# Kernel tuning notes

Measured on AMD Instinct MI355X. Metric: run time of the kernel, lower is better.

Reference implementation:

```python
import jax, jax.numpy as jnp
import numpy as np

B, H, L = 16, 512, 2048
N2 = 32  # d_state/2 complex modes
DT_MIN, DT_MAX = 1e-3, 1e-1


def setup_inputs() -> dict:
    key = jax.random.key(0)
    ks = jax.random.split(key, 8)
    u = jax.random.normal(ks[0], (B, H, L), dtype=jnp.float32)
    D = jax.random.normal(ks[1], (H,), dtype=jnp.float32)
    # log-uniform timescales in [DT_MIN, DT_MAX]
    r = jax.random.uniform(ks[2], (H,), dtype=jnp.float32)
    log_dt = (np.log(DT_MIN) + r * (np.log(DT_MAX) - np.log(DT_MIN))).astype(jnp.float32)
    C_re = jax.random.normal(ks[3], (H, N2), dtype=jnp.float32)
    C_im = jax.random.normal(ks[4], (H, N2), dtype=jnp.float32)
    W1 = jax.random.normal(ks[5], (L, 2 * H), dtype=jnp.float32) / np.float32(np.sqrt(L))
    b1 = jnp.zeros((2 * H,), dtype=jnp.float32)
    W2 = jax.random.normal(ks[6], (2 * H, H), dtype=jnp.float32) / np.float32(np.sqrt(2 * H))
    b2 = jnp.zeros((H,), dtype=jnp.float32)
    return {"u": u, "D": D, "log_dt": log_dt, "C_re": C_re, "C_im": C_im,
            "W1": W1, "b1": b1, "W2": W2, "b2": b2}


def _s4d_kernel(log_dt, C_re, C_im, length):
    # S4D-Lin: A_n = -1/2 + i*pi*n
    n = jnp.arange(N2, dtype=jnp.float32)
    A = -0.5 + 1j * jnp.pi * n                      # (N2,)
    dt = jnp.exp(log_dt)                             # (H,)
    dtA = dt[:, None] * A[None, :]                   # (H, N2)
    C = (C_re + 1j * C_im) * (jnp.exp(dtA) - 1.0) / A
    # Vandermonde: k[h, l] = 2 * Re sum_n C[h,n] * exp(dtA[h,n] * l)
    K = jnp.exp(dtA[:, :, None] * jnp.arange(length, dtype=jnp.float32))  # (H, N2, L)
    return 2.0 * jnp.einsum('hn,hnl->hl', C, K).real  # (H, L)


def reference(u, D, log_dt, C_re, C_im, W1, b1, W2, b2):
    # u: (B, H, L)
    k = _s4d_kernel(log_dt, C_re, C_im, L)           # (H, L)
    k_f = jnp.fft.rfft(k, n=2 * L, axis=-1)          # (H, L+1)
    u_f = jnp.fft.rfft(u, n=2 * L, axis=-1)          # (B, H, L+1)
    y = jnp.fft.irfft(u_f * k_f[None], n=2 * L, axis=-1)[..., :L]
    y = y + u * D[:, None]
    y = jax.nn.gelu(y, approximate=False)
    # keras Conv1D(k=1) / tanh / Dense applied to channels-first tensor:
    # dense over last axis L -> 2H, tanh, dense 2H -> H
    y = jnp.tanh(jnp.einsum('bhl,lf->bhf', y, W1) + b1)  # (B, H, 2H)
    y = jnp.einsum('bhf,fo->bho', y, W2) + b2            # (B, H, H)
    return y
```

## Files before the change

kernel.cpp:

```cpp
#include <hip/hip_runtime.h>
#include <math.h>

#define B_  16
#define H_  512
#define L_  2048
#define N2_ 32
#define NC_ 16
#define LC_ 128

typedef __attribute__((ext_vector_type(8))) short short8;
typedef __attribute__((ext_vector_type(4))) float f32x4;

__device__ __forceinline__ short f2bf(float x) {
    unsigned u = __builtin_bit_cast(unsigned, x);
    u += 0x7fffu + ((u >> 16) & 1u);
    return (short)(u >> 16);
}
__device__ __forceinline__ float bf2f(unsigned short s) {
    unsigned u = ((unsigned)s) << 16;
    return __builtin_bit_cast(float, u);
}

__global__ void k0_table(const float* __restrict__ log_dt,
                         const float* __restrict__ C_re,
                         const float* __restrict__ C_im,
                         float4* __restrict__ tab) {
    int idx = blockIdx.x * blockDim.x + threadIdx.x;
    if (idx >= H_ * N2_) return;
    int h = idx >> 5, n = idx & 31;
    float dt = expf(log_dt[h]);
    float e  = expf(-0.5f * dt);
    float th = 3.14159265358979323846f * (float)n * dt;
    float lr = e * cosf(th), li = e * sinf(th);
    float ar = -0.5f, ai = 3.14159265358979323846f * (float)n;
    float den = ar * ar + ai * ai;
    float x = lr - 1.0f, y = li;
    float nr = (x * ar + y * ai) / den;
    float ni = (y * ar - x * ai) / den;
    float cr = C_re[idx], ci = C_im[idx];
    tab[idx] = make_float4(lr, li, cr * nr - ci * ni, cr * ni + ci * nr);
}

__global__ void t0_pow(const float4* __restrict__ tab, float2* __restrict__ POW) {
    int t = blockIdx.x * 256 + threadIdx.x;
    if (t >= H_ * N2_) return;
    int h = t >> 5;
    float4 v = tab[t];
    float lr = v.x, li = v.y;
    float pr = 1.0f, pi = 0.0f;
    float2* base = POW + (size_t)h * 129 * N2_ + (t & 31);
    for (int m = 0; m <= 128; ++m) {
        base[(size_t)m * N2_] = make_float2(pr, pi);
        float npr = pr * lr - pi * li;
        float npi = pr * li + pi * lr;
        pr = npr; pi = npi;
    }
}

__global__ void t_ktab(const float4* __restrict__ tab, const float2* __restrict__ POW,
                       float* __restrict__ ktab) {
    int t = blockIdx.x * 256 + threadIdx.x;
    if (t >= H_ * 128) return;
    int h = t >> 7, m = t & 127;
    const float2* P = POW + (size_t)h * 129 * N2_ + (size_t)m * N2_;
    const float4* tb = tab + h * N2_;
    float s = 0.0f;
    for (int n = 0; n < N2_; ++n) {
        float2 p = P[n];
        float4 v = tb[n];
        s += v.z * p.x - v.w * p.y;
    }
    ktab[t] = 2.0f * s;
}

__global__ void __launch_bounds__(256)
t1_fill(const float4* __restrict__ tab, const float2* __restrict__ POW,
        const float* __restrict__ ktab, short* __restrict__ Psw,
        short* __restrict__ Vsw) {
    int t = blockIdx.x * 256 + threadIdx.x;
    int sub = t & 7;
    int rowg = t >> 3;
    int h = rowg / 320, row = rowg % 320;
    if (row < 192) {
        short8 s0, s1;
        if (row < 128) {
            int l = row;
#pragma unroll
            for (int mm = 0; mm < 8; ++mm) {
                int m0 = sub * 16 + mm, m1 = m0 + 8;
                s0[mm] = (m0 <= l) ? f2bf(ktab[h * 128 + (l - m0)]) : (short)0;
                s1[mm] = (m1 <= l) ? f2bf(ktab[h * 128 + (l - m1)]) : (short)0;
            }
        } else {
            int j = row - 128, nn = j >> 1, part = j & 1;
            const float2* P = POW + (size_t)h * 129 * N2_ + nn;
#pragma unroll
            for (int mm = 0; mm < 8; ++mm) {
                int m0 = sub * 16 + mm, m1 = m0 + 8;
                float2 p0 = P[(size_t)(127 - m0) * N2_];
                float2 p1 = P[(size_t)(127 - m1) * N2_];
                s0[mm] = f2bf(part ? p0.y : p0.x);
                s1[mm] = f2bf(part ? p1.y : p1.x);
            }
        }
        *(short8*)(Psw + ((size_t)(h * 16 + sub * 2 + 0) * 192 + row) * 8) = s0;
        *(short8*)(Psw + ((size_t)(h * 16 + sub * 2 + 1) * 192 + row) * 8) = s1;
    } else {
        int l = row - 192;
        const float2* P = POW + (size_t)h * 129 * N2_ + (size_t)(l + 1) * N2_;
        const float4* tb = tab + h * N2_;
        short8 s;
#pragma unroll
        for (int jj = 0; jj < 8; ++jj) {
            int j = sub * 8 + jj, nn = j >> 1;
            float2 p = P[nn];
            float4 cv = tb[nn];
            float re = cv.z * p.x - cv.w * p.y;
            float im = cv.z * p.y + cv.w * p.x;
            s[jj] = f2bf((j & 1) ? -2.0f * im : 2.0f * re);
        }
        *(short8*)(Vsw + ((size_t)(h * 8 + sub) * 128 + l) * 8) = s;
    }
}

__global__ void __launch_bounds__(256)
conv_mfma(const float* __restrict__ u, const short* __restrict__ Psw,
          float* __restrict__ E, short* __restrict__ Ybuf) {
    __shared__ short Ps[16 * 192 * 8];
    __shared__ short As[4 * 128 * 8];
    int h = blockIdx.x, mh = blockIdx.y;
    int tid = threadIdx.x;
    {
        const short8* Pg = (const short8*)(Psw + (size_t)h * 24576);
        short8* PsV = (short8*)Ps;
#pragma unroll
        for (int j = 0; j < 12; ++j) PsV[tid + j * 256] = Pg[tid + j * 256];
    }
    int row = tid >> 1, half = tid & 1;
    int R = mh * 128 + row, b = R >> 4, c = R & 15;
    const float* up = u + ((size_t)(b * H_ + h)) * L_ + (size_t)c * LC_ + half * 16;
    short8* AsV = (short8*)As;

    int lane = tid & 63, wave = tid >> 6;
    int wm = wave >> 1, wn = wave & 1;
    int lrow = lane & 15, lk = lane >> 4;
    const short8* AsF = (const short8*)As;
    const short8* PsF = (const short8*)Ps;

    f32x4 acc[4][6] = {};
    float4 fv0 = *(const float4*)(up + 0);
    float4 fv1 = *(const float4*)(up + 4);
    float4 fv2 = *(const float4*)(up + 8);
    float4 fv3 = *(const float4*)(up + 12);
    for (int ks = 0; ks < 4; ++ks) {
        __syncthreads();
        short8 s0, s1;
        s0[0] = f2bf(fv0.x); s0[1] = f2bf(fv0.y); s0[2] = f2bf(fv0.z); s0[3] = f2bf(fv0.w);
        s0[4] = f2bf(fv1.x); s0[5] = f2bf(fv1.y); s0[6] = f2bf(fv1.z); s0[7] = f2bf(fv1.w);
        s1[0] = f2bf(fv2.x); s1[1] = f2bf(fv2.y); s1[2] = f2bf(fv2.z); s1[3] = f2bf(fv2.w);
        s1[4] = f2bf(fv3.x); s1[5] = f2bf(fv3.y); s1[6] = f2bf(fv3.z); s1[7] = f2bf(fv3.w);
        AsV[(half * 2 + 0) * 128 + row] = s0;
        AsV[(half * 2 + 1) * 128 + row] = s1;
        __syncthreads();
        if (ks < 3) {
            const float* nx = up + (ks + 1) * 32;
            fv0 = *(const float4*)(nx + 0);
            fv1 = *(const float4*)(nx + 4);
            fv2 = *(const float4*)(nx + 8);
            fv3 = *(const float4*)(nx + 12);
        }
        short8 af[4], bfr[6];
#pragma unroll
        for (int m = 0; m < 4; ++m)
            af[m] = AsF[lk * 128 + wm * 64 + m * 16 + lrow];
#pragma unroll
        for (int n = 0; n < 6; ++n)
            bfr[n] = PsF[(ks * 4 + lk) * 192 + wn * 96 + n * 16 + lrow];
#pragma unroll
        for (int m = 0; m < 4; ++m)
#pragma unroll
            for (int n = 0; n < 6; ++n)
                acc[m][n] = __builtin_amdgcn_mfma_f32_16x16x32_bf16(
                    af[m], bfr[n], acc[m][n], 0, 0, 0);
    }
#pragma unroll
    for (int nf = 0; nf < 6; ++nf) {
        int col = wn * 96 + nf * 16 + lrow;
#pragma unroll
        for (int mf = 0; mf < 4; ++mf) {
            int rb = wm * 64 + mf * 16 + lk * 4;
#pragma unroll
            for (int r = 0; r < 4; ++r) {
                int rr = rb + r;
                int Rr = mh * 128 + rr, bb = Rr >> 4, cc = Rr & 15;
                float vv = acc[mf][nf][r];
                if (col < 128) {
                    Ybuf[((size_t)(bb * H_ + h)) * L_ + (size_t)cc * LC_ + col] = f2bf(vv);
                } else {
                    E[((size_t)(bb * H_ + h) * NC_ + cc) * 64 + (col - 128)] = vv;
                }
            }
        }
    }
}

__global__ void k2_scan(const float* __restrict__ log_dt, float2* __restrict__ ES) {
    int t = blockIdx.x * 256 + threadIdx.x;
    if (t >= B_ * H_ * N2_) return;
    int n  = t & 31;
    int h  = (t >> 5) & (H_ - 1);
    int bh = t >> 5;
    float dt = expf(log_dt[h]);
    float e  = expf(-0.5f * dt * (float)LC_);
    float th = 3.14159265358979323846f * (float)n * dt * (float)LC_;
    float Lr = e * cosf(th), Li = e * sinf(th);
    float cr = 0.0f, ci = 0.0f;
    float2* base = ES + (size_t)bh * NC_ * N2_ + n;
#pragma unroll
    for (int c = 0; c < NC_; ++c) {
        float2 Ev = base[(size_t)c * N2_];
        base[(size_t)c * N2_] = make_float2(cr, ci);
        float ncr = fmaf(Lr, cr, fmaf(-Li, ci, Ev.x));
        float nci = fmaf(Lr, ci, fmaf(Li, cr, Ev.y));
        cr = ncr; ci = nci;
    }
}

__global__ void __launch_bounds__(256)
dcarry_mfma(const float* __restrict__ ES, const short* __restrict__ Vsw,
            short* __restrict__ gbf) {
    __shared__ short Sa[8 * 128 * 8];
    __shared__ short Vb[8 * 128 * 8];
    int h = blockIdx.x, mh = blockIdx.y;
    int tid = threadIdx.x;
    {
        const short8* Vg = (const short8*)(Vsw + (size_t)h * 8192);
        short8* VbV = (short8*)Vb;
#pragma unroll
        for (int j = 0; j < 4; ++j) VbV[tid + j * 256] = Vg[tid + j * 256];
    }
    int row = tid >> 1, half = tid & 1;
    int R = mh * 128 + row, b = R >> 4, c = R & 15;
    {
        const float* sp = ES + ((size_t)(b * H_ + h) * NC_ + c) * 64 + half * 32;
        short8* SaV = (short8*)Sa;
#pragma unroll
        for (int gg = 0; gg < 4; ++gg) {
            float4 f0 = *(const float4*)(sp + gg * 8);
            float4 f1 = *(const float4*)(sp + gg * 8 + 4);
            short8 s;
            s[0] = f2bf(f0.x); s[1] = f2bf(f0.y); s[2] = f2bf(f0.z); s[3] = f2bf(f0.w);
            s[4] = f2bf(f1.x); s[5] = f2bf(f1.y); s[6] = f2bf(f1.z); s[7] = f2bf(f1.w);
            SaV[(half * 4 + gg) * 128 + row] = s;
        }
    }
    __syncthreads();
    int lane = tid & 63, wave = tid >> 6;
    int wm = wave >> 1, wn = wave & 1;
    int lrow = lane & 15, lk = lane >> 4;
    const short8* SaF = (const short8*)Sa;
    const short8* VbF = (const short8*)Vb;
    f32x4 acc[4][4] = {};
#pragma unroll
    for (int ks = 0; ks < 2; ++ks) {
        int g = ks * 4 + lk;
        short8 af[4], bf[4];
#pragma unroll
        for (int m = 0; m < 4; ++m)
            af[m] = SaF[g * 128 + wm * 64 + m * 16 + lrow];
#pragma unroll
        for (int n = 0; n < 4; ++n)
            bf[n] = VbF[g * 128 + wn * 64 + n * 16 + lrow];
#pragma unroll
        for (int m = 0; m < 4; ++m)
#pragma unroll
            for (int n = 0; n < 4; ++n)
                acc[m][n] = __builtin_amdgcn_mfma_f32_16x16x32_bf16(
                    af[m], bf[n], acc[m][n], 0, 0, 0);
    }
#pragma unroll
    for (int nf = 0; nf < 4; ++nf) {
        int l = wn * 64 + nf * 16 + lrow;
#pragma unroll
        for (int mf = 0; mf < 4; ++mf) {
            int rb = wm * 64 + mf * 16 + lk * 4;
#pragma unroll
            for (int r = 0; r < 4; ++r) {
                int Rr = mh * 128 + rb + r, bb = Rr >> 4, cc = Rr & 15;
                size_t gaddr = ((size_t)(bb * H_ + h)) * L_ + (size_t)cc * LC_ + l;
                gbf[gaddr] = f2bf(acc[mf][nf][r]);
            }
        }
    }
}

__global__ void __launch_bounds__(256)
egelu(const float* __restrict__ u, const float* __restrict__ Dv,
      const short* __restrict__ Ybuf, short* __restrict__ gbf) {
    size_t total = (size_t)B_ * H_ * L_ / 8;
    size_t stride = (size_t)gridDim.x * 256;
    for (size_t i = (size_t)blockIdx.x * 256 + threadIdx.x; i < total; i += stride) {
        size_t e = i * 8;
        int h = (int)((e >> 11) & (H_ - 1));
        float dv = Dv[h];
        short8 yv = *(const short8*)(Ybuf + e);
        short8 cv = *(const short8*)(gbf + e);
        float4 u0 = *(const float4*)(u + e);
        float4 u1 = *(const float4*)(u + e + 4);
        float uu[8] = {u0.x, u0.y, u0.z, u0.w, u1.x, u1.y, u1.z, u1.w};
        short8 o;
#pragma unroll
        for (int j = 0; j < 8; ++j) {
            float y = bf2f((unsigned short)yv[j]) + bf2f((unsigned short)cv[j]) + dv * uu[j];
            o[j] = f2bf(0.5f * y * (1.0f + erff(y * 0.70710678118654752f)));
        }
        *(short8*)(gbf + e) = o;
    }
}

__global__ void __launch_bounds__(256)
wtrans(const float* __restrict__ W, short* __restrict__ Wt, int K, int N) {
    __shared__ short tile[32][33];
    int bk = blockIdx.x * 32, bn = blockIdx.y * 32;
    int tx = threadIdx.x & 31, ty = threadIdx.x >> 5;
#pragma unroll
    for (int i = 0; i < 4; ++i)
        tile[ty + i * 8][tx] = f2bf(W[(size_t)(bk + ty + i * 8) * N + bn + tx]);
    __syncthreads();
#pragma unroll
    for (int i = 0; i < 4; ++i)
        Wt[(size_t)(bn + ty + i * 8) * K + bk + tx] = tile[tx][ty + i * 8];
}

template<bool TANH, bool OUTBF>
__global__ void __launch_bounds__(256)
gemm_mfma(const short* __restrict__ A, const short* __restrict__ Bt,
          const float* __restrict__ bias, void* __restrict__ Cout,
          int M, int N, int K) {
    __shared__ short As[4 * 128 * 8];
    __shared__ short Bs[4 * 128 * 8];
    int tid  = threadIdx.x;
    int lane = tid & 63;
    int wave = tid >> 6;
    int wm = wave >> 1, wn = wave & 1;
    int lrow = lane & 15, kblk = lane >> 4;
    int row0 = blockIdx.x * 128, col0 = blockIdx.y * 128;

    int srow = tid >> 2;
    int sk   = (tid & 3) * 8;
    const short* Ag0 = A  + (size_t)(row0 + srow) * K + sk;
    const short* Ag1 = A  + (size_t)(row0 + 64 + srow) * K + sk;
    const short* Bg0 = Bt + (size_t)(col0 + srow) * K + sk;
    const short* Bg1 = Bt + (size_t)(col0 + 64 + srow) * K + sk;
    int si0 = (tid & 3) * 1024 + srow * 8;
    int si1 = (tid & 3) * 1024 + (srow + 64) * 8;

    f32x4 acc[4][4] = {};
    short8 av0 = *(const short8*)Ag0, av1 = *(const short8*)Ag1;
    short8 bv0 = *(const short8*)Bg0, bv1 = *(const short8*)Bg1;

    for (int k0 = 0; k0 < K; k0 += 32) {
        __syncthreads();
        *(short8*)&As[si0] = av0;
        *(short8*)&As[si1] = av1;
        *(short8*)&Bs[si0] = bv0;
        *(short8*)&Bs[si1] = bv1;
        __syncthreads();
        if (k0 + 32 < K) {
            av0 = *(const short8*)(Ag0 + k0 + 32);
            av1 = *(const short8*)(Ag1 + k0 + 32);
            bv0 = *(const short8*)(Bg0 + k0 + 32);
            bv1 = *(const short8*)(Bg1 + k0 + 32);
        }
        short8 af[4], bf[4];
#pragma unroll
        for (int m = 0; m < 4; ++m)
            af[m] = *(const short8*)&As[kblk * 1024 + (wm * 64 + m * 16 + lrow) * 8];
#pragma unroll
        for (int n = 0; n < 4; ++n)
            bf[n] = *(const short8*)&Bs[kblk * 1024 + (wn * 64 + n * 16 + lrow) * 8];
#pragma unroll
        for (int m = 0; m < 4; ++m)
#pragma unroll
            for (int n = 0; n < 4; ++n)
                acc[m][n] = __builtin_amdgcn_mfma_f32_16x16x32_bf16(
                    af[m], bf[n], acc[m][n], 0, 0, 0);
    }
#pragma unroll
    for (int n = 0; n < 4; ++n) {
        int col = col0 + wn * 64 + n * 16 + lrow;
        float bb = bias[col];
#pragma unroll
        for (int m = 0; m < 4; ++m) {
            int rowb = row0 + wm * 64 + m * 16 + kblk * 4;
#pragma unroll
            for (int r = 0; r < 4; ++r) {
                float v = acc[m][n][r] + bb;
                if (TANH) v = tanhf(v);
                if (OUTBF) ((short*)Cout)[(size_t)(rowb + r) * N + col] = f2bf(v);
                else       ((float*)Cout)[(size_t)(rowb + r) * N + col] = v;
            }
        }
    }
}

extern "C" void kernel_launch(void* const* d_in, const int* in_sizes, int n_in,
                              void* d_out, int out_size, void* d_ws, size_t ws_size,
                              hipStream_t stream) {
    const float* u     = (const float*)d_in[0];
    const float* D     = (const float*)d_in[1];
    const float* logdt = (const float*)d_in[2];
    const float* C_re  = (const float*)d_in[3];
    const float* C_im  = (const float*)d_in[4];
    const float* W1    = (const float*)d_in[5];
    const float* b1    = (const float*)d_in[6];
    const float* W2    = (const float*)d_in[7];
    const float* b2    = (const float*)d_in[8];
    float* out = (float*)d_out;

    char* p = (char*)d_ws;
    float4* tab = (float4*)p;            p += 262144;
    char* regionA = p;                   p += 33554432;
    float2* POW  = (float2*)regionA;
    float*  ktab = (float*)(regionA + 16908288);
    short*  Ybuf = (short*)regionA;
    short* Psw = (short*)p;              p += 25165824;
    short* Vsw = (short*)p;              p += 8388608;
    float* E   = (float*)p;              p += 33554432;
    short* gbf = (short*)p;              p += 33554432;
    short* tb  = (short*)p;              p += 16777216;
    short* w1t = (short*)p;              p += 4194304;
    short* w2t = (short*)p;

    k0_table<<<H_ * N2_ / 256, 256, 0, stream>>>(logdt, C_re, C_im, tab);
    t0_pow  <<<H_ * N2_ / 256, 256, 0, stream>>>(tab, POW);
    t_ktab  <<<H_ * 128 / 256, 256, 0, stream>>>(tab, POW, ktab);
    t1_fill <<<H_ * 320 * 8 / 256, 256, 0, stream>>>(tab, POW, ktab, Psw, Vsw);
    wtrans  <<<dim3(L_ / 32, 2 * H_ / 32), 256, 0, stream>>>(W1, w1t, L_, 2 * H_);
    wtrans  <<<dim3(2 * H_ / 32, H_ / 32), 256, 0, stream>>>(W2, w2t, 2 * H_, H_);

    conv_mfma  <<<dim3(H_, 2), 256, 0, stream>>>(u, Psw, E, Ybuf);
    k2_scan    <<<B_ * H_ * N2_ / 256, 256, 0, stream>>>(logdt, (float2*)E);
    dcarry_mfma<<<dim3(H_, 2), 256, 0, stream>>>(E, Vsw, gbf);
    egelu      <<<2048, 256, 0, stream>>>(u, D, Ybuf, gbf);

    gemm_mfma<true, true ><<<dim3(B_ * H_ / 128, 2 * H_ / 128), 256, 0, stream>>>(
        gbf, w1t, b1, tb, B_ * H_, 2 * H_, L_);
    gemm_mfma<false, false><<<dim3(B_ * H_ / 128, H_ / 128), 256, 0, stream>>>(
        tb, w2t, b2, out, B_ * H_, H_, 2 * H_);
}
```

Before: 223.0 us.

## Double-depth register prefetch and padded row-major LDS tiles in bf16 MFMA GEMM

The GEMM main loop now keeps two sets of prefetch registers, so global loads are issued two K-tiles ahead; the loop is unrolled by two through a lambda to alternate between the sets. The shared-memory tiles also move from a k-block-major layout to row-major rows padded to a 36-short stride, which is meant to avoid bank conflicts. The aim is to hide more global-load latency behind the MFMAs. In exchange it uses more registers, assumes K is a multiple of 64, and the 72-byte row stride leaves the 16-byte LDS reads unaligned, which may split them into narrower accesses.

```diff
diff --git a/kernel.cpp b/kernel.cpp
--- a/kernel.cpp
+++ b/kernel.cpp
@@ -337,8 +337,8 @@
 gemm_mfma(const short* __restrict__ A, const short* __restrict__ Bt,
           const float* __restrict__ bias, void* __restrict__ Cout,
           int M, int N, int K) {
-    __shared__ short As[4 * 128 * 8];
-    __shared__ short Bs[4 * 128 * 8];
+    __shared__ short As[128 * 36 + 16];
+    __shared__ short Bs[128 * 36 + 16];
     int tid  = threadIdx.x;
     int lane = tid & 63;
     int wave = tid >> 6;
@@ -352,40 +352,51 @@
     const short* Ag1 = A  + (size_t)(row0 + 64 + srow) * K + sk;
     const short* Bg0 = Bt + (size_t)(col0 + srow) * K + sk;
     const short* Bg1 = Bt + (size_t)(col0 + 64 + srow) * K + sk;
-    int si0 = (tid & 3) * 1024 + srow * 8;
-    int si1 = (tid & 3) * 1024 + (srow + 64) * 8;
+    int si0 = srow * 36 + sk;
+    int si1 = (srow + 64) * 36 + sk;
 
     f32x4 acc[4][4] = {};
-    short8 av0 = *(const short8*)Ag0, av1 = *(const short8*)Ag1;
-    short8 bv0 = *(const short8*)Bg0, bv1 = *(const short8*)Bg1;
-
-    for (int k0 = 0; k0 < K; k0 += 32) {
+    const int NT = K >> 5;
+
+    short8 xa0 = *(const short8*)(Ag0),      xa1 = *(const short8*)(Ag1);
+    short8 xb0 = *(const short8*)(Bg0),      xb1 = *(const short8*)(Bg1);
+    short8 ya0 = *(const short8*)(Ag0 + 32), ya1 = *(const short8*)(Ag1 + 32);
+    short8 yb0 = *(const short8*)(Bg0 + 32), yb1 = *(const short8*)(Bg1 + 32);
+
+    auto gstep = [&](short8& A0, short8& A1, short8& B0, short8& B1, int tnext) {
         __syncthreads();
-        *(short8*)&As[si0] = av0;
-        *(short8*)&As[si1] = av1;
-        *(short8*)&Bs[si0] = bv0;
-        *(short8*)&Bs[si1] = bv1;
+        *(short8*)&As[si0] = A0;
+        *(short8*)&As[si1] = A1;
+        *(short8*)&Bs[si0] = B0;
+        *(short8*)&Bs[si1] = B1;
         __syncthreads();
-        if (k0 + 32 < K) {
-            av0 = *(const short8*)(Ag0 + k0 + 32);
-            av1 = *(const short8*)(Ag1 + k0 + 32);
-            bv0 = *(const short8*)(Bg0 + k0 + 32);
-            bv1 = *(const short8*)(Bg1 + k0 + 32);
+        if (tnext < NT) {
+            int ko = tnext << 5;
+            A0 = *(const short8*)(Ag0 + ko);
+            A1 = *(const short8*)(Ag1 + ko);
+            B0 = *(const short8*)(Bg0 + ko);
+            B1 = *(const short8*)(Bg1 + ko);
         }
         short8 af[4], bf[4];
 #pragma unroll
         for (int m = 0; m < 4; ++m)
-            af[m] = *(const short8*)&As[kblk * 1024 + (wm * 64 + m * 16 + lrow) * 8];
+            af[m] = *(const short8*)&As[(wm * 64 + m * 16 + lrow) * 36 + kblk * 8];
 #pragma unroll
         for (int n = 0; n < 4; ++n)
-            bf[n] = *(const short8*)&Bs[kblk * 1024 + (wn * 64 + n * 16 + lrow) * 8];
+            bf[n] = *(const short8*)&Bs[(wn * 64 + n * 16 + lrow) * 36 + kblk * 8];
 #pragma unroll
         for (int m = 0; m < 4; ++m)
 #pragma unroll
             for (int n = 0; n < 4; ++n)
                 acc[m][n] = __builtin_amdgcn_mfma_f32_16x16x32_bf16(
                     af[m], bf[n], acc[m][n], 0, 0, 0);
-    }
+    };
+
+    for (int t = 0; t < NT; t += 2) {
+        gstep(xa0, xa1, xb0, xb1, t + 2);
+        gstep(ya0, ya1, yb0, yb1, t + 3);
+    }
+
 #pragma unroll
     for (int n = 0; n < 4; ++n) {
         int col = col0 + wn * 64 + n * 16 + lrow;
```

Result: faster. 207.3 us (-7.0%).
